# Optimization experiments

Hardware: AMD Instinct MI355X
Metric: run time of the kernel (lower is better)

Reference implementation:

```python
import jax, jax.numpy as jnp
import numpy as np

T, B, D = 256, 256, 512
H, DK = 8, 64          # num_heads, d_kv; inner_dim = H*DK = 512
NUM_GROUPS = 16


def setup_inputs() -> dict:
    key = jax.random.key(0)
    ks = jax.random.split(key, 6)
    hidden_states = jax.random.normal(ks[0], (T, B, D), dtype=jnp.float32)
    # sorted group ids over the batch axis (what _infer_group_ids_from_mask recovers)
    group_ids = jnp.sort(jax.random.randint(ks[1], (B,), 0, NUM_GROUPS, dtype=jnp.int32))
    scale = 1.0 / np.sqrt(D)
    Wq = jax.random.normal(ks[2], (D, H * DK), dtype=jnp.float32) * scale
    Wk = jax.random.normal(ks[3], (D, H * DK), dtype=jnp.float32) * scale
    Wv = jax.random.normal(ks[4], (D, H * DK), dtype=jnp.float32) * scale
    Wo = jax.random.normal(ks[5], (H * DK, D), dtype=jnp.float32) * scale
    return {"hidden_states": hidden_states, "group_ids": group_ids,
            "Wq": Wq, "Wk": Wk, "Wv": Wv, "Wo": Wo}


def reference(hidden_states, group_ids, Wq, Wk, Wv, Wo):
    # Group-restricted self-attention along the batch axis, per time step & head.
    # Equivalent to the block-sparse MiniFlash kernel: entries attend only to
    # batch entries with the same group id.
    t, b, d = hidden_states.shape
    q = (hidden_states @ Wq).reshape(t, b, H, DK)
    k = (hidden_states @ Wk).reshape(t, b, H, DK)
    v = (hidden_states @ Wv).reshape(t, b, H, DK)
    sm_scale = 1.0 / np.sqrt(DK)
    # scores: [T, H, B, B] over the batch axis
    scores = jnp.einsum("tihd,tjhd->thij", q, k) * sm_scale
    allowed = group_ids[:, None] == group_ids[None, :]          # [B, B]
    neg = jnp.finfo(scores.dtype).min
    scores = jnp.where(allowed[None, None, :, :], scores, neg)
    attn = jax.nn.softmax(scores, axis=-1)
    out = jnp.einsum("thij,tjhd->tihd", attn, v).reshape(t, b, H * DK)
    return out @ Wo
```

## Files before the change

### kernel.cpp

```cpp
#include <hip/hip_runtime.h>
#include <hip/hip_bf16.h>

typedef __attribute__((ext_vector_type(8))) short short8;
typedef __attribute__((ext_vector_type(4))) short short4v;
typedef __attribute__((ext_vector_type(4))) float f32x4;

#define MFMA16(a, b, c) __builtin_amdgcn_mfma_f32_16x16x32_bf16(a, b, c, 0, 0, 0)

__device__ __forceinline__ unsigned short f2bf(float f) {
    union { __hip_bfloat16 h; unsigned short u; } v;
    v.h = __float2bfloat16(f);
    return v.u;
}

__device__ __forceinline__ short8 pack8(float4 a, float4 b) {
    short8 p;
    p[0] = (short)f2bf(a.x); p[1] = (short)f2bf(a.y);
    p[2] = (short)f2bf(a.z); p[3] = (short)f2bf(a.w);
    p[4] = (short)f2bf(b.x); p[5] = (short)f2bf(b.y);
    p[6] = (short)f2bf(b.z); p[7] = (short)f2bf(b.w);
    return p;
}

__device__ __forceinline__ int swz64(int row, int bytecol) {
    return row * 64 + ((bytecol ^ ((row & 7) << 4)) >> 1);
}
__device__ __forceinline__ int swz256(int row, int bytecol) {
    return row * 256 + ((bytecol ^ ((row & 7) << 4)) >> 1);
}
__device__ __forceinline__ int swz32(int row, int bytecol) {
    return row * 32 + ((bytecol ^ ((row & 3) << 4)) >> 1);
}

__device__ __forceinline__ void async16(void* lds_uniform, const void* gsrc) {
    __builtin_amdgcn_global_load_lds(
        (const __attribute__((address_space(1))) unsigned int*)gsrc,
        (__attribute__((address_space(3))) unsigned int*)lds_uniform,
        16, 0, 0);
}

__global__ __launch_bounds__(256) void wprep(
    const float* __restrict__ Wq, const float* __restrict__ Wk,
    const float* __restrict__ Wv, const float* __restrict__ Wo,
    unsigned short* __restrict__ wt, int swz)
{
    __shared__ float tile[64][65];
    const int bid = blockIdx.x;
    const int m = bid >> 6, tb = bid & 63;
    const int kr = (tb >> 3) << 6, nc = (tb & 7) << 6;
    const float* W = (m == 0) ? Wq : (m == 1) ? Wk : (m == 2) ? Wv : Wo;
    const int tid = threadIdx.x;
    for (int i = tid; i < 4096; i += 256)
        tile[i >> 6][i & 63] = W[(size_t)(kr + (i >> 6)) * 512 + nc + (i & 63)];
    __syncthreads();
    unsigned short* dst = wt + (size_t)m * 262144;
    for (int i = tid; i < 4096; i += 256) {
        const int n = nc + (i >> 6);
        const int e = i & 63;
        const int rsw = swz ? ((n & 7) * 8) : 0;
        dst[(size_t)n * 512 + kr + e] = f2bf(tile[e ^ rsw][i >> 6]);
    }
}

__global__ __launch_bounds__(256) void xprep(
    const float* __restrict__ hs, unsigned short* __restrict__ xb)
{
    const long long total = 4194304;
    for (long long g = (long long)blockIdx.x * 256 + threadIdx.x; g < total;
         g += (long long)gridDim.x * 256) {
        const int row = (int)(g >> 6);
        const int e0  = ((int)g & 63) * 8;
        const int src = e0 ^ ((row & 7) * 8);
        const float* s = hs + (size_t)row * 512 + src;
        const float4 f0 = *(const float4*)s;
        const float4 f1 = *(const float4*)(s + 4);
        *(short8*)(xb + (size_t)row * 512 + e0) = pack8(f0, f1);
    }
}

template<int F32OUT>
__global__ __launch_bounds__(512, 2) void gemm256(
    const unsigned short* __restrict__ A,
    const unsigned short* __restrict__ B,
    unsigned short* __restrict__ obf,
    float* __restrict__ of32,
    int nbcnt)
{
    __shared__ unsigned short Ash[2][256 * 64];
    __shared__ unsigned short Bsh[3][256 * 64];

    const int orig  = blockIdx.x;
    const int chunk = gridDim.x >> 3;
    const int wg = (orig & 7) * chunk + (orig >> 3);
    const int mb = wg / nbcnt;
    const int nb = wg - mb * nbcnt;

    const int tid  = threadIdx.x;
    const int lane = tid & 63;
    const int w    = tid >> 6;
    const int l15  = lane & 15;
    const int hi4  = lane >> 4;
    const int wr   = w >> 2;
    const int wc   = w & 3;

    f32x4 acc[8][4];
    #pragma unroll
    for (int m = 0; m < 8; ++m)
        #pragma unroll
        for (int n = 0; n < 4; ++n)
            acc[m][n] = (f32x4){0.f, 0.f, 0.f, 0.f};

    const char* __restrict__ Ab = (const char*)(A + (size_t)mb * 256 * 512);
    const char* __restrict__ Bb = (const char*)(B + (size_t)nb * 256 * 512);

    auto STAGE_A = [&](int buf, int kt, int j2) {
        #pragma unroll
        for (int j = 0; j < 2; ++j) {
            const int c = w * 4 + j2 * 2 + j;
            const int sbyte = c * 1024;
            const int s = sbyte + lane * 16;
            const int row = s >> 7, colb = s & 127;
            async16((char*)&Ash[buf][0] + sbyte,
                    Ab + (size_t)row * 1024 + (size_t)kt * 128 + colb);
        }
    };
    auto STAGE_B = [&](int buf, int kt, int j2) {
        #pragma unroll
        for (int j = 0; j < 2; ++j) {
            const int c = w * 4 + j2 * 2 + j;
            const int sbyte = c * 1024;
            const int s = sbyte + lane * 16;
            const int row = s >> 7, colb = s & 127;
            async16((char*)&Bsh[buf][0] + sbyte,
                    Bb + (size_t)row * 1024 + (size_t)kt * 128 + colb);
        }
    };

    STAGE_A(0, 0, 0); STAGE_A(0, 0, 1);
    STAGE_B(0, 0, 0); STAGE_B(0, 0, 1);
    STAGE_B(1, 1, 0); STAGE_B(1, 1, 1);
    asm volatile("s_waitcnt vmcnt(4)" ::: "memory");
    __builtin_amdgcn_s_barrier();

    short8 bfr[4][2];

    for (int t = 0; t < 8; ++t) {
        const int ab = t & 1;
        const int bb = t % 3;
        #pragma unroll
        for (int p = 0; p < 4; ++p) {
            short8 af[2][2];
            #pragma unroll
            for (int mi = 0; mi < 2; ++mi) {
                const int row = wr * 128 + (p * 2 + mi) * 16 + l15;
                af[mi][0] = *(const short8*)&Ash[ab][swz64(row, hi4 * 16)];
                af[mi][1] = *(const short8*)&Ash[ab][swz64(row, 64 + hi4 * 16)];
            }
            if (p == 0) {
                #pragma unroll
                for (int nt = 0; nt < 4; ++nt) {
                    const int col = wc * 64 + nt * 16 + l15;
                    bfr[nt][0] = *(const short8*)&Bsh[bb][swz64(col, hi4 * 16)];
                    bfr[nt][1] = *(const short8*)&Bsh[bb][swz64(col, 64 + hi4 * 16)];
                }
            }
            if (p < 2) { if (t < 7) STAGE_A(ab ^ 1, t + 1, p); }
            else       { if (t < 6) STAGE_B((t + 2) % 3, t + 2, p - 2); }

            __builtin_amdgcn_s_barrier();
            __builtin_amdgcn_s_setprio(1);
            #pragma unroll
            for (int nt = 0; nt < 4; ++nt) {
                #pragma unroll
                for (int mi = 0; mi < 2; ++mi) {
                    const int m = p * 2 + mi;
                    acc[m][nt] = MFMA16(af[mi][0], bfr[nt][0], acc[m][nt]);
                    acc[m][nt] = MFMA16(af[mi][1], bfr[nt][1], acc[m][nt]);
                }
            }
            __builtin_amdgcn_s_setprio(0);
            if (p < 3) __builtin_amdgcn_s_barrier();
        }
        if (t < 7) {
            if (t < 6) asm volatile("s_waitcnt vmcnt(4)" ::: "memory");
            else       asm volatile("s_waitcnt vmcnt(0)" ::: "memory");
            __builtin_amdgcn_s_barrier();
        }
    }

    #pragma unroll
    for (int m = 0; m < 8; ++m) {
        #pragma unroll
        for (int nt = 0; nt < 4; ++nt) {
            const int colt = nb * 256 + wc * 64 + nt * 16 + l15;
            #pragma unroll
            for (int r = 0; r < 4; ++r) {
                const int row = mb * 256 + wr * 128 + m * 16 + hi4 * 4 + r;
                if (F32OUT) {
                    of32[(size_t)row * 512 + colt] = acc[m][nt][r];
                } else {
                    const int mat = colt >> 9, cc = colt & 511;
                    obf[(size_t)mat * 33554432 + (size_t)row * 512 + cc] =
                        f2bf(acc[m][nt][r]);
                }
            }
        }
    }
}

__global__ __launch_bounds__(512, 4) void attn_split(
    unsigned short* __restrict__ qkvb,
    const int* __restrict__ gid,
    int doswz)
{
    __shared__ unsigned short Vt[64 * 256];
    __shared__ unsigned short Ps[256 * 32];

    const int th = blockIdx.x;
    const int t = th >> 3, h = th & 7;
    const int tid  = threadIdx.x;
    const int lane = tid & 63;
    const int w    = tid >> 6;
    const int l15  = lane & 15;
    const int hi4  = lane >> 4;
    const int wrow = w << 5;

    const size_t rowbase = (size_t)t * 256 * 512 + h * 64;
    unsigned short* __restrict__ qb = qkvb + rowbase;
    const unsigned short* __restrict__ kbp = qkvb + 33554432ull + rowbase;
    const unsigned short* __restrict__ vbp = qkvb + 67108864ull + rowbase;

    {
        const int d2 = (tid & 31) * 2;
        const int jg = tid >> 5;
        unsigned int vv[16];
        #pragma unroll
        for (int jj = 0; jj < 16; ++jj)
            vv[jj] = *(const unsigned int*)(vbp + (size_t)(jg * 16 + jj) * 512 + d2);
        short8 a0, a1, b0, b1;
        #pragma unroll
        for (int jj = 0; jj < 8; ++jj) {
            a0[jj] = (short)(vv[jj] & 0xFFFFu);
            b0[jj] = (short)(vv[jj] >> 16);
            a1[jj] = (short)(vv[8 + jj] & 0xFFFFu);
            b1[jj] = (short)(vv[8 + jj] >> 16);
        }
        *(short8*)&Vt[swz256(d2,     jg * 32)]      = a0;
        *(short8*)&Vt[swz256(d2,     jg * 32 + 16)] = a1;
        *(short8*)&Vt[swz256(d2 + 1, jg * 32)]      = b0;
        *(short8*)&Vt[swz256(d2 + 1, jg * 32 + 16)] = b1;
    }
    short8 qf[2][2];
    #pragma unroll
    for (int a = 0; a < 2; ++a)
        #pragma unroll
        for (int ks = 0; ks < 2; ++ks)
            qf[a][ks] = *(const short8*)(qb + (size_t)(wrow + a * 16 + l15) * 512 +
                                          ks * 32 + hi4 * 8);

    int rg[2][4];
    #pragma unroll
    for (int a = 0; a < 2; ++a)
        #pragma unroll
        for (int r = 0; r < 4; ++r)
            rg[a][r] = gid[wrow + a * 16 + hi4 * 4 + r];
    const int gfirst = gid[wrow], glast = gid[wrow + 31];
    int lo = 0, hi2 = 256;
    while (lo < hi2) { const int mid = (lo + hi2) >> 1;
        if (gid[mid] < gfirst) lo = mid + 1; else hi2 = mid; }
    const int klo = lo;
    lo = 0; hi2 = 256;
    while (lo < hi2) { const int mid = (lo + hi2) >> 1;
        if (gid[mid] <= glast) lo = mid + 1; else hi2 = mid; }
    const int khi = lo - 1;

    __syncthreads();

    f32x4 o[2][4];
    float mrun[2][4], lrun[2][4];
    #pragma unroll
    for (int a = 0; a < 2; ++a)
        #pragma unroll
        for (int n = 0; n < 4; ++n)
            o[a][n] = (f32x4){0.f, 0.f, 0.f, 0.f};
    #pragma unroll
    for (int a = 0; a < 2; ++a)
        #pragma unroll
        for (int r = 0; r < 4; ++r) { mrun[a][r] = -3.0e38f; lrun[a][r] = 0.f; }

    for (int kc = klo & ~31; kc <= khi; kc += 32) {
        f32x4 sfr[2][2];
        __builtin_amdgcn_s_setprio(1);
        #pragma unroll
        for (int n = 0; n < 2; ++n) {
            const unsigned short* krp = kbp + (size_t)(kc + n * 16 + l15) * 512;
            const short8 kf0 = *(const short8*)(krp + hi4 * 8);
            const short8 kf1 = *(const short8*)(krp + 32 + hi4 * 8);
            #pragma unroll
            for (int a = 0; a < 2; ++a) {
                f32x4 z = (f32x4){0.f, 0.f, 0.f, 0.f};
                z = MFMA16(qf[a][0], kf0, z);
                z = MFMA16(qf[a][1], kf1, z);
                sfr[a][n] = z;
            }
        }
        __builtin_amdgcn_s_setprio(0);
        int cg[2];
        #pragma unroll
        for (int n = 0; n < 2; ++n) cg[n] = gid[kc + n * 16 + l15];

        #pragma unroll
        for (int a = 0; a < 2; ++a) {
            #pragma unroll
            for (int r = 0; r < 4; ++r) {
                const int gr = rg[a][r];
                float sv[2];
                float smax = -3.0e38f;
                #pragma unroll
                for (int n = 0; n < 2; ++n) {
                    float x = sfr[a][n][r] * 0.125f;
                    x = (cg[n] == gr) ? x : -3.0e38f;
                    sv[n] = x;
                    smax = fmaxf(smax, x);
                }
                smax = fmaxf(smax, __shfl_xor(smax, 1));
                smax = fmaxf(smax, __shfl_xor(smax, 2));
                smax = fmaxf(smax, __shfl_xor(smax, 4));
                smax = fmaxf(smax, __shfl_xor(smax, 8));
                const float newm = fmaxf(mrun[a][r], smax);
                const float corr = __expf(mrun[a][r] - newm);
                float ps = 0.f;
                unsigned short pb[2];
                #pragma unroll
                for (int n = 0; n < 2; ++n) {
                    const float p = (sv[n] > -1.0e38f) ? __expf(sv[n] - newm) : 0.f;
                    ps += p;
                    pb[n] = f2bf(p);
                }
                ps += __shfl_xor(ps, 1); ps += __shfl_xor(ps, 2);
                ps += __shfl_xor(ps, 4); ps += __shfl_xor(ps, 8);
                lrun[a][r] = lrun[a][r] * corr + ps;
                mrun[a][r] = newm;
                #pragma unroll
                for (int n = 0; n < 4; ++n) o[a][n][r] *= corr;
                const int prow = wrow + a * 16 + hi4 * 4 + r;
                #pragma unroll
                for (int n = 0; n < 2; ++n)
                    Ps[swz32(prow, (n * 16 + l15) * 2)] = pb[n];
            }
        }

        __builtin_amdgcn_s_setprio(1);
        #pragma unroll
        for (int a = 0; a < 2; ++a) {
            const short8 pa = *(const short8*)&Ps[swz32(wrow + a * 16 + l15, hi4 * 16)];
            #pragma unroll
            for (int n = 0; n < 4; ++n) {
                const short8 vb = *(const short8*)&Vt[swz256(n * 16 + l15,
                                                             (kc + hi4 * 8) * 2)];
                o[a][n] = MFMA16(pa, vb, o[a][n]);
            }
        }
        __builtin_amdgcn_s_setprio(0);
    }

    #pragma unroll
    for (int a = 0; a < 2; ++a) {
        #pragma unroll
        for (int r = 0; r < 4; ++r) {
            const int row = wrow + a * 16 + hi4 * 4 + r;
            const float inv = 1.0f / lrun[a][r];
            const int rsw = doswz ? ((row & 7) * 8) : 0;
            #pragma unroll
            for (int n = 0; n < 4; ++n) {
                const int cc = n * 16 + l15;
                qb[(size_t)row * 512 + (cc ^ rsw)] = f2bf(o[a][n][r] * inv);
            }
        }
    }
}

__global__ __launch_bounds__(1024, 4) void qkv_gemm2(
    const float* __restrict__ hs,
    const unsigned short* __restrict__ wt,
    unsigned short* __restrict__ qkvb)
{
    __shared__ unsigned short As[128 * 64];
    __shared__ unsigned short Bts[512 * 64];

    const int orig = blockIdx.x;
    const int wg = (orig & 7) * 192 + (orig >> 3);
    const int mb = wg / 3;
    const int nb = wg - mb * 3;

    const int tid  = threadIdx.x;
    const int lane = tid & 63;
    const int w    = tid >> 6;
    const int l15  = lane & 15;
    const int hi4  = lane >> 4;
    const int wr   = w >> 3;
    const int wc   = w & 7;

    f32x4 acc[4][4];
    #pragma unroll
    for (int mt = 0; mt < 4; ++mt)
        #pragma unroll
        for (int nt = 0; nt < 4; ++nt)
            acc[mt][nt] = (f32x4){0.f, 0.f, 0.f, 0.f};

    const int ar = tid >> 3, aq = tid & 7;
    const int bc = tid >> 1, bh = tid & 1;
    const float* __restrict__ asrc = hs + ((size_t)mb * 128 + ar) * 512 + aq * 8;
    const unsigned short* __restrict__ bsrc =
        wt + ((size_t)nb * 512 + bc) * 512 + bh * 32;

    float4 a0, a1;
    short8 b8[4];
    a0 = *(const float4*)asrc;
    a1 = *(const float4*)(asrc + 4);
    #pragma unroll
    for (int q = 0; q < 4; ++q) b8[q] = *(const short8*)(bsrc + q * 8);

    for (int kb = 0; kb < 512; kb += 64) {
        *(short8*)&As[swz64(ar, aq * 16)] = pack8(a0, a1);
        #pragma unroll
        for (int q = 0; q < 4; ++q)
            *(short8*)&Bts[swz64(bc, bh * 64 + q * 16)] = b8[q];
        __syncthreads();
        if (kb < 448) {
            const int kn = kb + 64;
            a0 = *(const float4*)(asrc + kn);
            a1 = *(const float4*)(asrc + kn + 4);
            #pragma unroll
            for (int q = 0; q < 4; ++q)
                b8[q] = *(const short8*)(bsrc + kn + q * 8);
        }
        #pragma unroll
        for (int ks = 0; ks < 2; ++ks) {
            short8 af[4];
            #pragma unroll
            for (int mt = 0; mt < 4; ++mt)
                af[mt] = *(const short8*)&As[swz64(wr * 64 + mt * 16 + l15,
                                                   ks * 64 + hi4 * 16)];
            __builtin_amdgcn_s_setprio(1);
            #pragma unroll
            for (int nt = 0; nt < 4; ++nt) {
                const short8 bf = *(const short8*)&Bts[swz64(wc * 64 + nt * 16 + l15,
                                                             ks * 64 + hi4 * 16)];
                #pragma unroll
                for (int mt = 0; mt < 4; ++mt)
                    acc[mt][nt] = MFMA16(af[mt], bf, acc[mt][nt]);
            }
            __builtin_amdgcn_s_setprio(0);
        }
        __syncthreads();
    }

    unsigned short* __restrict__ dst = qkvb + (size_t)nb * 33554432ull;
    #pragma unroll
    for (int mt = 0; mt < 4; ++mt) {
        #pragma unroll
        for (int nt = 0; nt < 4; ++nt) {
            const int col = wc * 64 + nt * 16 + l15;
            #pragma unroll
            for (int r = 0; r < 4; ++r) {
                const int row = mb * 128 + wr * 64 + mt * 16 + hi4 * 4 + r;
                dst[(size_t)row * 512 + col] = f2bf(acc[mt][nt][r]);
            }
        }
    }
}

__global__ __launch_bounds__(1024, 4) void qkv_attn_mfma(
    const float* __restrict__ hs,
    const int*   __restrict__ gid,
    const float* __restrict__ Wq, const float* __restrict__ Wk,
    const float* __restrict__ Wv,
    float*       __restrict__ out)
{
    __shared__ unsigned short Xs[256 * 64];
    __shared__ unsigned short Wsh[192 * 64];
    __shared__ unsigned short Ksh[256 * 64];
    __shared__ unsigned short Vt[64 * 256];
    __shared__ unsigned short XP[256 * 64];
    __shared__ int sgid[256];
    __shared__ int glo[16], ghi[16];

    const int bid = blockIdx.x;
    const int h   = (bid & 63) >> 3;
    const int t   = ((bid >> 6) << 3) + (bid & 7);

    const int tid  = threadIdx.x;
    const int lane = tid & 63;
    const int w    = tid >> 6;
    const int l15  = lane & 15;
    const int hi4  = lane >> 4;
    const int mg   = w & 3;
    const int ng   = w >> 2;

    if (tid < 16) { glo[tid] = 256; ghi[tid] = -1; }
    __syncthreads();
    if (tid < 256) {
        const int g = gid[tid];
        sgid[tid] = g;
        atomicMin(&glo[g], tid);
        atomicMax(&ghi[g], tid);
    }

    const float* __restrict__ Xbase = hs + (size_t)t * (256 * 512);

    const int xr = tid >> 2, xq = tid & 3;
    const bool doW = tid < 768;
    const int wc = tid >> 2;
    const int wq = tid & 3;
    const int wmat = wc >> 6, wcol = wc & 63;
    const float* __restrict__ wfsrc =
        (wmat == 0) ? Wq : (wmat == 1) ? Wk : Wv;

    f32x4 acc[4][3];
    #pragma unroll
    for (int mt = 0; mt < 4; ++mt)
        #pragma unroll
        for (int nt = 0; nt < 3; ++nt)
            acc[mt][nt] = (f32x4){0.f, 0.f, 0.f, 0.f};

    float4 xf[4];
    short8 w8[2];
    {
        const float* s = Xbase + (size_t)xr * 512 + xq * 16;
        xf[0] = *(const float4*)(s + 0);  xf[1] = *(const float4*)(s + 4);
        xf[2] = *(const float4*)(s + 8);  xf[3] = *(const float4*)(s + 12);
        if (doW) {
            #pragma unroll
            for (int b = 0; b < 2; ++b)
                #pragma unroll
                for (int j = 0; j < 8; ++j)
                    w8[b][j] = (short)f2bf(
                        wfsrc[(size_t)(wq * 16 + b * 8 + j) * 512 + h * 64 + wcol]);
        }
    }

    for (int kb = 0; kb < 512; kb += 64) {
        *(short8*)&Xs[swz64(xr, xq * 32 + 0)]  = pack8(xf[0], xf[1]);
        *(short8*)&Xs[swz64(xr, xq * 32 + 16)] = pack8(xf[2], xf[3]);
        if (doW) {
            *(short8*)&Wsh[swz64(wc, wq * 32 + 0)]  = w8[0];
            *(short8*)&Wsh[swz64(wc, wq * 32 + 16)] = w8[1];
        }
        __syncthreads();
        if (kb < 448) {
            const int kn = kb + 64;
            const float* s = Xbase + (size_t)xr * 512 + kn + xq * 16;
            xf[0] = *(const float4*)(s + 0);  xf[1] = *(const float4*)(s + 4);
            xf[2] = *(const float4*)(s + 8);  xf[3] = *(const float4*)(s + 12);
            if (doW) {
                #pragma unroll
                for (int b = 0; b < 2; ++b)
                    #pragma unroll
                    for (int j = 0; j < 8; ++j)
                        w8[b][j] = (short)f2bf(
                            wfsrc[(size_t)(kn + wq * 16 + b * 8 + j) * 512 + h * 64 + wcol]);
            }
        }
        #pragma unroll
        for (int ks = 0; ks < 2; ++ks) {
            short8 af[4];
            #pragma unroll
            for (int mt = 0; mt < 4; ++mt)
                af[mt] = *(const short8*)&Xs[swz64(mg * 64 + mt * 16 + l15,
                                                   ks * 64 + hi4 * 16)];
            __builtin_amdgcn_s_setprio(1);
            #pragma unroll
            for (int nt = 0; nt < 3; ++nt) {
                const short8 bf = *(const short8*)&Wsh[swz64(ng * 48 + nt * 16 + l15,
                                                             ks * 64 + hi4 * 16)];
                #pragma unroll
                for (int mt = 0; mt < 4; ++mt)
                    acc[mt][nt] = MFMA16(af[mt], bf, acc[mt][nt]);
            }
            __builtin_amdgcn_s_setprio(0);
        }
        __syncthreads();
    }

    #pragma unroll
    for (int nt = 0; nt < 3; ++nt) {
        const int c0 = (ng * 3 + nt) * 16;
        const int m  = c0 >> 6;
        const int d0 = c0 & 63;
        #pragma unroll
        for (int mt = 0; mt < 4; ++mt) {
            const int rowb = mg * 64 + mt * 16 + hi4 * 4;
            if (m == 0) {
                #pragma unroll
                for (int r = 0; r < 4; ++r)
                    XP[swz64(rowb + r, (d0 + l15) * 2)] = f2bf(acc[mt][nt][r]);
            } else if (m == 1) {
                #pragma unroll
                for (int r = 0; r < 4; ++r)
                    Ksh[swz64(rowb + r, (d0 + l15) * 2)] = f2bf(acc[mt][nt][r]);
            } else {
                short4v vv;
                #pragma unroll
                for (int r = 0; r < 4; ++r) vv[r] = (short)f2bf(acc[mt][nt][r]);
                *(short4v*)&Vt[swz256(d0 + l15, rowb * 2)] = vv;
            }
        }
    }
    __syncthreads();

    const int wrow = w << 4;
    int rg[4];
    #pragma unroll
    for (int r = 0; r < 4; ++r) rg[r] = sgid[wrow + hi4 * 4 + r];
    const int klo = glo[sgid[wrow]];
    const int khi = ghi[sgid[wrow + 15]];

    short8 qf[2];
    #pragma unroll
    for (int ks = 0; ks < 2; ++ks)
        qf[ks] = *(const short8*)&XP[swz64(wrow + l15, ks * 64 + hi4 * 16)];

    f32x4 o[4];
    float mrun[4], lrun[4];
    #pragma unroll
    for (int n = 0; n < 4; ++n) o[n] = (f32x4){0.f, 0.f, 0.f, 0.f};
    #pragma unroll
    for (int r = 0; r < 4; ++r) { mrun[r] = -3.0e38f; lrun[r] = 0.f; }

    for (int kc = klo & ~63; kc <= khi; kc += 64) {
        f32x4 sfr[4];
        __builtin_amdgcn_s_setprio(1);
        #pragma unroll
        for (int n = 0; n < 4; ++n) {
            const int krow = kc + n * 16 + l15;
            const short8 kf0 = *(const short8*)&Ksh[swz64(krow, hi4 * 16)];
            const short8 kf1 = *(const short8*)&Ksh[swz64(krow, 64 + hi4 * 16)];
            f32x4 z = (f32x4){0.f, 0.f, 0.f, 0.f};
            z = MFMA16(qf[0], kf0, z);
            z = MFMA16(qf[1], kf1, z);
            sfr[n] = z;
        }
        __builtin_amdgcn_s_setprio(0);
        int cg[4];
        #pragma unroll
        for (int n = 0; n < 4; ++n) cg[n] = sgid[kc + n * 16 + l15];

        #pragma unroll
        for (int r = 0; r < 4; ++r) {
            const int gr = rg[r];
            float sv[4];
            float smax = -3.0e38f;
            #pragma unroll
            for (int n = 0; n < 4; ++n) {
                float x = sfr[n][r] * 0.125f;
                x = (cg[n] == gr) ? x : -3.0e38f;
                sv[n] = x;
                smax = fmaxf(smax, x);
            }
            smax = fmaxf(smax, __shfl_xor(smax, 1));
            smax = fmaxf(smax, __shfl_xor(smax, 2));
            smax = fmaxf(smax, __shfl_xor(smax, 4));
            smax = fmaxf(smax, __shfl_xor(smax, 8));
            const float newm = fmaxf(mrun[r], smax);
            const float corr = __expf(mrun[r] - newm);
            float ps = 0.f;
            unsigned short pb[4];
            #pragma unroll
            for (int n = 0; n < 4; ++n) {
                const float p = (sv[n] > -1.0e38f) ? __expf(sv[n] - newm) : 0.f;
                ps += p;
                pb[n] = f2bf(p);
            }
            ps += __shfl_xor(ps, 1); ps += __shfl_xor(ps, 2);
            ps += __shfl_xor(ps, 4); ps += __shfl_xor(ps, 8);
            lrun[r] = lrun[r] * corr + ps;
            mrun[r] = newm;
            #pragma unroll
            for (int n = 0; n < 4; ++n) o[n][r] *= corr;
            const int prow = wrow + hi4 * 4 + r;
            #pragma unroll
            for (int n = 0; n < 4; ++n)
                XP[swz64(prow, (n * 16 + l15) * 2)] = pb[n];
        }

        const short8 pa0 = *(const short8*)&XP[swz64(wrow + l15, hi4 * 16)];
        const short8 pa1 = *(const short8*)&XP[swz64(wrow + l15, 64 + hi4 * 16)];
        __builtin_amdgcn_s_setprio(1);
        #pragma unroll
        for (int n = 0; n < 4; ++n) {
            const short8 vb0 = *(const short8*)&Vt[swz256(n * 16 + l15, (kc + hi4 * 8) * 2)];
            const short8 vb1 = *(const short8*)&Vt[swz256(n * 16 + l15, (kc + 32 + hi4 * 8) * 2)];
            o[n] = MFMA16(pa0, vb0, o[n]);
            o[n] = MFMA16(pa1, vb1, o[n]);
        }
        __builtin_amdgcn_s_setprio(0);
    }

    float* __restrict__ op = out + (size_t)t * (256 * 512) + h * 64;
    #pragma unroll
    for (int r = 0; r < 4; ++r) {
        const int row = wrow + hi4 * 4 + r;
        const float inv = 1.0f / lrun[r];
        #pragma unroll
        for (int n = 0; n < 4; ++n)
            op[(size_t)row * 512 + n * 16 + l15] = o[n][r] * inv;
    }
}

__global__ __launch_bounds__(1024, 4) void oproj_mfma(
    const float* __restrict__ Wo,
    const unsigned short* __restrict__ wot,
    const unsigned short* __restrict__ abuf,
    float* __restrict__ out)
{
    __shared__ unsigned short As[128 * 40];
    __shared__ unsigned short Bts[512 * 40];

    const int tid  = threadIdx.x;
    const int lane = tid & 63;
    const int w    = tid >> 6;
    const int l15  = lane & 15;
    const int hi4  = lane >> 4;
    const int wr   = w >> 2;
    const int wc   = w & 3;
    const size_t r0 = (size_t)blockIdx.x * 128;

    f32x4 acc[2][8];
    #pragma unroll
    for (int m = 0; m < 2; ++m)
        #pragma unroll
        for (int n = 0; n < 8; ++n)
            acc[m][n] = (f32x4){0.f, 0.f, 0.f, 0.f};

    const bool isA = tid < 512;
    const int bn = tid & 511;
    const int ai = bn >> 2, aq = bn & 3;

    float4 af0, af1;
    short8 a8;
    short8 b8[4];

    if (isA) {
        if (abuf) {
            a8 = *(const short8*)(abuf + (r0 + ai) * 512 + aq * 8);
        } else {
            const float* s = out + (r0 + ai) * 512 + aq * 8;
            af0 = *(const float4*)s; af1 = *(const float4*)(s + 4);
        }
    } else {
        if (wot) {
            #pragma unroll
            for (int q = 0; q < 4; ++q)
                b8[q] = *(const short8*)(wot + (size_t)bn * 512 + q * 8);
        } else {
            #pragma unroll
            for (int q = 0; q < 4; ++q)
                #pragma unroll
                for (int j = 0; j < 8; ++j)
                    b8[q][j] = (short)f2bf(Wo[(size_t)(q * 8 + j) * 512 + bn]);
        }
    }

    for (int kb = 0; kb < 512; kb += 32) {
        if (isA) *(short8*)&As[ai * 40 + aq * 8] = abuf ? a8 : pack8(af0, af1);
        else {
            #pragma unroll
            for (int q = 0; q < 4; ++q)
                *(short8*)&Bts[bn * 40 + q * 8] = b8[q];
        }
        __syncthreads();
        if (kb < 480) {
            const int kn = kb + 32;
            if (isA) {
                if (abuf) {
                    a8 = *(const short8*)(abuf + (r0 + ai) * 512 + kn + aq * 8);
                } else {
                    const float* s = out + (r0 + ai) * 512 + kn + aq * 8;
                    af0 = *(const float4*)s; af1 = *(const float4*)(s + 4);
                }
            } else {
                if (wot) {
                    #pragma unroll
                    for (int q = 0; q < 4; ++q)
                        b8[q] = *(const short8*)(wot + (size_t)bn * 512 + kn + q * 8);
                } else {
                    #pragma unroll
                    for (int q = 0; q < 4; ++q)
                        #pragma unroll
                        for (int j = 0; j < 8; ++j)
                            b8[q][j] = (short)f2bf(Wo[(size_t)(kn + q * 8 + j) * 512 + bn]);
                }
            }
        }
        short8 afr[2];
        #pragma unroll
        for (int m = 0; m < 2; ++m)
            afr[m] = *(const short8*)&As[(wr * 32 + m * 16 + l15) * 40 + hi4 * 8];
        __builtin_amdgcn_s_setprio(1);
        #pragma unroll
        for (int n = 0; n < 8; ++n) {
            const short8 bfr = *(const short8*)&Bts[(wc * 128 + n * 16 + l15) * 40 + hi4 * 8];
            #pragma unroll
            for (int m = 0; m < 2; ++m)
                acc[m][n] = MFMA16(afr[m], bfr, acc[m][n]);
        }
        __builtin_amdgcn_s_setprio(0);
        __syncthreads();
    }

    #pragma unroll
    for (int m = 0; m < 2; ++m)
        #pragma unroll
        for (int n = 0; n < 8; ++n)
            #pragma unroll
            for (int r = 0; r < 4; ++r)
                out[(r0 + wr * 32 + m * 16 + hi4 * 4 + r) * 512 + wc * 128 + n * 16 + l15] =
                    acc[m][n][r];
}

extern "C" void kernel_launch(void* const* d_in, const int* in_sizes, int n_in,
                              void* d_out, int out_size, void* d_ws, size_t ws_size,
                              hipStream_t stream) {
    const float* hs  = (const float*)d_in[0];
    const int*   gid = (const int*)  d_in[1];
    const float* Wq  = (const float*)d_in[2];
    const float* Wk  = (const float*)d_in[3];
    const float* Wv  = (const float*)d_in[4];
    const float* Wo  = (const float*)d_in[5];
    float* outp = (float*)d_out;

    const size_t WT_S  = 1048576;
    const size_t XB_S  = 33554432;
    const size_t QKV_S = 100663296;
    unsigned short* wt = (unsigned short*)d_ws;
    unsigned short* wot = wt + (size_t)3 * 262144;

    if (ws_size >= (WT_S + XB_S + QKV_S) * 2) {
        unsigned short* xb   = wt + WT_S;
        unsigned short* qkvb = xb + XB_S;
        wprep<<<256, 256, 0, stream>>>(Wq, Wk, Wv, Wo, wt, 1);
        xprep<<<2048, 256, 0, stream>>>(hs, xb);
        gemm256<0><<<1536, 512, 0, stream>>>(xb, wt, qkvb, nullptr, 6);
        attn_split<<<2048, 512, 0, stream>>>(qkvb, gid, 1);
        gemm256<1><<<512, 512, 0, stream>>>(qkvb, wot, nullptr, outp, 2);
    } else if (ws_size >= (WT_S + QKV_S) * 2) {
        unsigned short* qkvb = wt + WT_S;
        wprep<<<256, 256, 0, stream>>>(Wq, Wk, Wv, Wo, wt, 0);
        qkv_gemm2<<<1536, 1024, 0, stream>>>(hs, wt, qkvb);
        attn_split<<<2048, 512, 0, stream>>>(qkvb, gid, 0);
        oproj_mfma<<<512, 1024, 0, stream>>>(Wo, wot, qkvb, outp);
    } else {
        qkv_attn_mfma<<<2048, 1024, 0, stream>>>(hs, gid, Wq, Wk, Wv, outp);
        oproj_mfma<<<512, 1024, 0, stream>>>(Wo, nullptr, nullptr, outp);
    }
}
```

Baseline: 332.4 us.

## Write V transposed per (t,h) from projection GEMM epilogue, drop LDS transpose in attention

The QKV projection epilogues now store the V matrix directly in a transposed [t][h][d][batch] layout in global memory, using 4-wide vector stores. The attention kernel then reads V fragments straight from global memory instead of staging and transposing V through shared memory. This removes the per-block V load, the in-register shuffle, the LDS stores and a block-wide barrier. In exchange the MFMA V operands become global loads that may have higher latency, and the epilogue stores are strided.

New measurement: 347.9 us. +4.7%, slower.

```diff
diff --git a/kernel.cpp b/kernel.cpp
--- a/kernel.cpp
+++ b/kernel.cpp
@@ -25,11 +25,11 @@
 __device__ __forceinline__ int swz64(int row, int bytecol) {
     return row * 64 + ((bytecol ^ ((row & 7) << 4)) >> 1);
 }
+__device__ __forceinline__ int swz32(int row, int bytecol) {
+    return row * 32 + ((bytecol ^ ((row & 3) << 4)) >> 1);
+}
 __device__ __forceinline__ int swz256(int row, int bytecol) {
     return row * 256 + ((bytecol ^ ((row & 7) << 4)) >> 1);
-}
-__device__ __forceinline__ int swz32(int row, int bytecol) {
-    return row * 32 + ((bytecol ^ ((row & 3) << 4)) >> 1);
 }
 
 __device__ __forceinline__ void async16(void* lds_uniform, const void* gsrc) {
@@ -188,23 +188,48 @@
         }
     }
 
-    #pragma unroll
-    for (int m = 0; m < 8; ++m) {
-        #pragma unroll
-        for (int nt = 0; nt < 4; ++nt) {
-            const int colt = nb * 256 + wc * 64 + nt * 16 + l15;
-            #pragma unroll
-            for (int r = 0; r < 4; ++r) {
-                const int row = mb * 256 + wr * 128 + m * 16 + hi4 * 4 + r;
-                if (F32OUT) {
+    if (F32OUT) {
+        #pragma unroll
+        for (int m = 0; m < 8; ++m)
+            #pragma unroll
+            for (int nt = 0; nt < 4; ++nt) {
+                const int colt = nb * 256 + wc * 64 + nt * 16 + l15;
+                #pragma unroll
+                for (int r = 0; r < 4; ++r) {
+                    const int row = mb * 256 + wr * 128 + m * 16 + hi4 * 4 + r;
                     of32[(size_t)row * 512 + colt] = acc[m][nt][r];
-                } else {
-                    const int mat = colt >> 9, cc = colt & 511;
+                }
+            }
+    } else if ((nb >> 1) == 2) {
+        unsigned short* __restrict__ vtb = obf + 67108864ull;
+        const int tt = mb;
+        #pragma unroll
+        for (int m = 0; m < 8; ++m) {
+            const int i0 = wr * 128 + m * 16 + hi4 * 4;
+            #pragma unroll
+            for (int nt = 0; nt < 4; ++nt) {
+                const int cc = (nb & 1) * 256 + wc * 64 + nt * 16 + l15;
+                const int h = cc >> 6, d = cc & 63;
+                short4v vv;
+                #pragma unroll
+                for (int r = 0; r < 4; ++r) vv[r] = (short)f2bf(acc[m][nt][r]);
+                *(short4v*)(vtb + (((size_t)tt * 8 + h) * 64 + d) * 256 + i0) = vv;
+            }
+        }
+    } else {
+        #pragma unroll
+        for (int m = 0; m < 8; ++m)
+            #pragma unroll
+            for (int nt = 0; nt < 4; ++nt) {
+                const int colt = nb * 256 + wc * 64 + nt * 16 + l15;
+                const int mat = colt >> 9, cc = colt & 511;
+                #pragma unroll
+                for (int r = 0; r < 4; ++r) {
+                    const int row = mb * 256 + wr * 128 + m * 16 + hi4 * 4 + r;
                     obf[(size_t)mat * 33554432 + (size_t)row * 512 + cc] =
                         f2bf(acc[m][nt][r]);
                 }
             }
-        }
     }
 }
 
@@ -213,7 +238,6 @@
     const int* __restrict__ gid,
     int doswz)
 {
-    __shared__ unsigned short Vt[64 * 256];
     __shared__ unsigned short Ps[256 * 32];
 
     const int th = blockIdx.x;
@@ -228,28 +252,8 @@
     const size_t rowbase = (size_t)t * 256 * 512 + h * 64;
     unsigned short* __restrict__ qb = qkvb + rowbase;
     const unsigned short* __restrict__ kbp = qkvb + 33554432ull + rowbase;
-    const unsigned short* __restrict__ vbp = qkvb + 67108864ull + rowbase;
-
-    {
-        const int d2 = (tid & 31) * 2;
-        const int jg = tid >> 5;
-        unsigned int vv[16];
-        #pragma unroll
-        for (int jj = 0; jj < 16; ++jj)
-            vv[jj] = *(const unsigned int*)(vbp + (size_t)(jg * 16 + jj) * 512 + d2);
-        short8 a0, a1, b0, b1;
-        #pragma unroll
-        for (int jj = 0; jj < 8; ++jj) {
-            a0[jj] = (short)(vv[jj] & 0xFFFFu);
-            b0[jj] = (short)(vv[jj] >> 16);
-            a1[jj] = (short)(vv[8 + jj] & 0xFFFFu);
-            b1[jj] = (short)(vv[8 + jj] >> 16);
-        }
-        *(short8*)&Vt[swz256(d2,     jg * 32)]      = a0;
-        *(short8*)&Vt[swz256(d2,     jg * 32 + 16)] = a1;
-        *(short8*)&Vt[swz256(d2 + 1, jg * 32)]      = b0;
-        *(short8*)&Vt[swz256(d2 + 1, jg * 32 + 16)] = b1;
-    }
+    const unsigned short* __restrict__ vtp = qkvb + 67108864ull + (size_t)th * 16384;
+
     short8 qf[2][2];
     #pragma unroll
     for (int a = 0; a < 2; ++a)
@@ -273,8 +277,6 @@
     while (lo < hi2) { const int mid = (lo + hi2) >> 1;
         if (gid[mid] <= glast) lo = mid + 1; else hi2 = mid; }
     const int khi = lo - 1;
-
-    __syncthreads();
 
     f32x4 o[2][4];
     float mrun[2][4], lrun[2][4];
@@ -356,8 +358,8 @@
             const short8 pa = *(const short8*)&Ps[swz32(wrow + a * 16 + l15, hi4 * 16)];
             #pragma unroll
             for (int n = 0; n < 4; ++n) {
-                const short8 vb = *(const short8*)&Vt[swz256(n * 16 + l15,
-                                                             (kc + hi4 * 8) * 2)];
+                const short8 vb = *(const short8*)(vtp + (size_t)(n * 16 + l15) * 256 +
+                                                    kc + hi4 * 8);
                 o[a][n] = MFMA16(pa, vb, o[a][n]);
             }
         }
@@ -456,16 +458,34 @@
         __syncthreads();
     }
 
-    unsigned short* __restrict__ dst = qkvb + (size_t)nb * 33554432ull;
-    #pragma unroll
-    for (int mt = 0; mt < 4; ++mt) {
-        #pragma unroll
-        for (int nt = 0; nt < 4; ++nt) {
-            const int col = wc * 64 + nt * 16 + l15;
-            #pragma unroll
-            for (int r = 0; r < 4; ++r) {
-                const int row = mb * 128 + wr * 64 + mt * 16 + hi4 * 4 + r;
-                dst[(size_t)row * 512 + col] = f2bf(acc[mt][nt][r]);
+    if (nb == 2) {
+        unsigned short* __restrict__ vtb = qkvb + 67108864ull;
+        const int tt = mb >> 1;
+        #pragma unroll
+        for (int mt = 0; mt < 4; ++mt) {
+            const int i0 = (mb & 1) * 128 + wr * 64 + mt * 16 + hi4 * 4;
+            #pragma unroll
+            for (int nt = 0; nt < 4; ++nt) {
+                const int col = wc * 64 + nt * 16 + l15;
+                const int h = col >> 6, d = col & 63;
+                short4v vv;
+                #pragma unroll
+                for (int r = 0; r < 4; ++r) vv[r] = (short)f2bf(acc[mt][nt][r]);
+                *(short4v*)(vtb + (((size_t)tt * 8 + h) * 64 + d) * 256 + i0) = vv;
+            }
+        }
+    } else {
+        unsigned short* __restrict__ dst = qkvb + (size_t)nb * 33554432ull;
+        #pragma unroll
+        for (int mt = 0; mt < 4; ++mt) {
+            #pragma unroll
+            for (int nt = 0; nt < 4; ++nt) {
+                const int col = wc * 64 + nt * 16 + l15;
+                #pragma unroll
+                for (int r = 0; r < 4; ++r) {
+                    const int row = mb * 128 + wr * 64 + mt * 16 + hi4 * 4 + r;
+                    dst[(size_t)row * 512 + col] = f2bf(acc[mt][nt][r]);
+                }
             }
         }
     }
```
